# Kernel tuning notes

Measured on AMD Instinct MI355X. Metric: run time of the kernel, lower is better.

## Reference

```python
import jax, jax.numpy as jnp
import numpy as np
from jax.scipy.special import gammaln

BIG_NEG = -1e9
MAX_K = 20  # args.sm_max_span_length


def setup_inputs() -> dict:
    key = jax.random.key(0)
    ks = jax.random.split(key, 7)
    B, N, d, C = 16, 2048, 256, 128
    features = jax.random.normal(ks[0], (B, N, d), dtype=jnp.float32)
    lengths = jax.random.randint(ks[1], (B,), N // 2, N + 1)
    gaussian_means = jax.random.normal(ks[2], (C, d), dtype=jnp.float32)
    cov_diag = jax.random.uniform(ks[3], (d,), minval=0.5, maxval=1.5, dtype=jnp.float32)
    transition_logits = jax.random.normal(ks[4], (C, C), dtype=jnp.float32)
    init_logits = jax.random.uniform(ks[5], (C,), dtype=jnp.float32)
    poisson_log_rates = jax.random.normal(ks[6], (C,), dtype=jnp.float32) * 0.5 + 1.5
    return {"features": features, "lengths": lengths, "gaussian_means": gaussian_means,
            "cov_diag": cov_diag, "transition_logits": transition_logits,
            "init_logits": init_logits, "poisson_log_rates": poisson_log_rates}


def _emission_log_probs(features, means, cov_diag):
    # Diagonal-covariance MultivariateNormal log-prob, one class per column.
    # Quadratic form expanded to avoid materializing [B,N,C,d].
    inv_var = 1.0 / cov_diag
    d = features.shape[-1]
    const = -0.5 * (d * jnp.log(2.0 * jnp.pi) + jnp.sum(jnp.log(cov_diag)))
    xq = jnp.einsum('bnd,d->bn', features * features, inv_var)          # [B,N]
    mq = jnp.einsum('cd,d->c', means * means, inv_var)                  # [C]
    xm = jnp.einsum('bnd,cd->bnc', features, means * inv_var)           # [B,N,C]
    return const - 0.5 * (xq[..., None] + mq[None, None, :] - 2.0 * xm)  # [B,N,C]


def _length_log_probs(log_rates, K):
    # Poisson log-prob for span lengths k = 1..K.
    ks = jnp.arange(1, K + 1, dtype=jnp.float32)[:, None]               # [K,1]
    return ks * log_rates[None, :] - jnp.exp(log_rates)[None, :] - gammaln(ks + 1.0)  # [K,C]


def _transition_log_probs(transition_logits):
    C = transition_logits.shape[0]
    masked = jnp.where(jnp.eye(C, dtype=bool), BIG_NEG, transition_logits)  # no self-transitions
    return jax.nn.log_softmax(masked, axis=0)  # normalized over destination class (dim 0)


def _semimarkov_logZ(emis_lp, lengths, init_lp, trans_lp, len_lp, K):
    # Segmental (semi-Markov) CRF forward algorithm with sliding-window span sums.
    B, N, C = emis_lp.shape
    cum = jnp.concatenate([jnp.zeros((B, 1, C), emis_lp.dtype), jnp.cumsum(emis_lp, axis=1)], axis=1)
    cum_pad = jnp.concatenate([jnp.zeros((B, K, C), emis_lp.dtype), cum], axis=1)  # idx t+K <-> position t
    beta0 = jnp.full((B, N + 1 + K, C), BIG_NEG, emis_lp.dtype)
    beta0 = beta0.at[:, K, :].set(init_lp[None, :])  # position 0: initial distribution
    len_rev = len_lp[::-1]  # len_rev[j] == length log-prob of span length K-j

    def step(beta, t):
        w = jax.lax.dynamic_slice(beta, (0, t, 0), (B, K, C))        # beta at positions t-K..t-1
        cw = jax.lax.dynamic_slice(cum_pad, (0, t, 0), (B, K, C))
        ct = jax.lax.dynamic_slice(cum_pad, (0, t + K, 0), (B, 1, C))
        span = w + len_rev[None, :, :] + (ct - cw)                    # [B,K,C] span scores ending at t
        alpha_t = jax.nn.logsumexp(span, axis=1)                      # [B,C]
        beta_t = jax.nn.logsumexp(alpha_t[:, None, :] + trans_lp[None, :, :], axis=2)  # to-class
        beta = jax.lax.dynamic_update_slice(beta, beta_t[:, None, :], (0, t + K, 0))
        return beta, alpha_t

    _, alphas = jax.lax.scan(step, beta0, jnp.arange(1, N + 1))       # alphas: [N,B,C]
    final = alphas[lengths - 1, jnp.arange(B)]                        # [B,C] at each sequence end
    return jax.nn.logsumexp(final, axis=1)                            # [B] log partition


def reference(features, lengths, gaussian_means, cov_diag, transition_logits, init_logits, poisson_log_rates):
    emis_lp = _emission_log_probs(features, gaussian_means, cov_diag)
    init_lp = jax.nn.log_softmax(init_logits, axis=0)
    trans_lp = _transition_log_probs(transition_logits)
    len_lp = _length_log_probs(poisson_log_rates, MAX_K)
    return _semimarkov_logZ(emis_lp, lengths, init_lp, trans_lp, len_lp, MAX_K)
```

## Files before the change

### kernel.cpp

```cpp
#include <hip/hip_runtime.h>
#include <math.h>

#define Bb 16
#define Nn 2048
#define Dd 256
#define Cc 128
#define Kk 20
#define BIG_NEG -1.0e9f

#define WS_EMIS   0
#define WS_MSC    (WS_EMIS + Bb*Nn*Cc)
#define WS_XQ     (WS_MSC + Cc*Dd)
#define WS_ECHAN  (WS_XQ + Bb*Nn)
#define WS_T      (WS_ECHAN + Cc)
#define WS_LEN    (WS_T + Cc*Cc)
#define WS_INIT   (WS_LEN + Kk*Cc)
#define WS_IVAR   (WS_INIT + Cc)

typedef __attribute__((ext_vector_type(8))) short short8;
typedef __attribute__((ext_vector_type(4))) float float4v;

__device__ __forceinline__ unsigned short f32_to_bf16(float x) {
  unsigned int u = __builtin_bit_cast(unsigned int, x);
  u = (u + 0x7FFFu + ((u >> 16) & 1u)) >> 16;
  return (unsigned short)u;
}

#define DPP_STEP(x, op, ctrl, rmask)                                          \
  do {                                                                        \
    int _yi = __builtin_amdgcn_update_dpp(                                    \
        __builtin_bit_cast(int, x), __builtin_bit_cast(int, x), ctrl, rmask,  \
        0xF, true);                                                           \
    x = op(x, __builtin_bit_cast(float, _yi));                                \
  } while (0)

__device__ __forceinline__ float dpp_add(float a, float b) { return a + b; }

__device__ __forceinline__ float wave_max64(float x) {
  DPP_STEP(x, fmaxf, 0xB1, 0xF);
  DPP_STEP(x, fmaxf, 0x4E, 0xF);
  DPP_STEP(x, fmaxf, 0x141, 0xF);
  DPP_STEP(x, fmaxf, 0x140, 0xF);
  DPP_STEP(x, fmaxf, 0x142, 0xA);
  DPP_STEP(x, fmaxf, 0x143, 0xC);
  return __builtin_bit_cast(float,
      __builtin_amdgcn_readlane(__builtin_bit_cast(int, x), 63));
}

__device__ __forceinline__ float wave_sum64(float x) {
  DPP_STEP(x, dpp_add, 0xB1, 0xF);
  DPP_STEP(x, dpp_add, 0x4E, 0xF);
  DPP_STEP(x, dpp_add, 0x141, 0xF);
  DPP_STEP(x, dpp_add, 0x140, 0xF);
  DPP_STEP(x, dpp_add, 0x142, 0xA);
  DPP_STEP(x, dpp_add, 0x143, 0xC);
  return __builtin_bit_cast(float,
      __builtin_amdgcn_readlane(__builtin_bit_cast(int, x), 63));
}

__global__ void prep_kernel(const float* __restrict__ means,
                            const float* __restrict__ cov,
                            const float* __restrict__ tl,
                            const float* __restrict__ il,
                            const float* __restrict__ plr,
                            float* __restrict__ ws) {
  __shared__ float s_iv[Dd];
  __shared__ float s_red[4];
  __shared__ float s_tlse[Cc];
  int tid = threadIdx.x;

  float cv = cov[tid];
  float iv = 1.0f / cv;
  s_iv[tid] = iv;
  ws[WS_IVAR + tid] = iv;
  float lg = __logf(cv);
  #pragma unroll
  for (int off = 1; off < 64; off <<= 1) lg += __shfl_xor(lg, off, 64);
  if ((tid & 63) == 0) s_red[tid >> 6] = lg;
  __syncthreads();
  float logdet = s_red[0] + s_red[1] + s_red[2] + s_red[3];
  float cconst = -0.5f * ((float)Dd * 1.8378770664093453f + logdet);

  unsigned short* mscb = (unsigned short*)(ws + WS_MSC);
  for (int idx = tid; idx < Cc * Dd; idx += 256) {
    int d = idx & (Dd - 1);
    mscb[idx] = f32_to_bf16(means[idx] * s_iv[d]);
  }
  if (tid < Cc) {
    float acc = 0.0f;
    for (int d = 0; d < Dd; d++) {
      float m = means[tid * Dd + d];
      acc = fmaf(m * m, s_iv[d], acc);
    }
    ws[WS_ECHAN + tid] = cconst - 0.5f * acc;
  }
  for (int idx = tid; idx < Kk * Cc; idx += 256) {
    int L = idx / Cc + 1;
    int c = idx & (Cc - 1);
    float r = plr[c];
    ws[WS_LEN + idx] = (float)L * r - __expf(r) - lgammaf((float)(L + 1));
  }

  __syncthreads();
  float x = (tid < Cc) ? il[tid] : -INFINITY;
  float mx = x;
  #pragma unroll
  for (int off = 1; off < 64; off <<= 1) mx = fmaxf(mx, __shfl_xor(mx, off, 64));
  if ((tid & 63) == 0) s_red[tid >> 6] = mx;
  __syncthreads();
  float M = fmaxf(s_red[0], s_red[1]);
  float se = (tid < Cc) ? __expf(x - M) : 0.0f;
  #pragma unroll
  for (int off = 1; off < 64; off <<= 1) se += __shfl_xor(se, off, 64);
  __syncthreads();
  if ((tid & 63) == 0) s_red[tid >> 6] = se;
  __syncthreads();
  float lse = M + __logf(s_red[0] + s_red[1]);
  if (tid < Cc) ws[WS_INIT + tid] = x - lse;

  if (tid < Cc) {
    int j = tid;
    float m2 = -INFINITY;
    for (int i = 0; i < Cc; i++) if (i != j) m2 = fmaxf(m2, tl[i * Cc + j]);
    float s2 = 0.0f;
    for (int i = 0; i < Cc; i++) if (i != j) s2 += __expf(tl[i * Cc + j] - m2);
    s_tlse[j] = m2 + __logf(s2);
  }
  __syncthreads();
  for (int idx = tid; idx < Cc * Cc; idx += 256) {
    int i = idx / Cc;
    int j = idx & (Cc - 1);
    ws[WS_T + idx] = (i == j) ? 0.0f : __expf(tl[idx] - s_tlse[j]);
  }
}

__global__ void xq_kernel(const float* __restrict__ f, float* __restrict__ ws) {
  int pos = blockIdx.x * 4 + (threadIdx.x >> 6);
  int lane = threadIdx.x & 63;
  const float4 fv = *(const float4*)&f[(size_t)pos * Dd + lane * 4];
  const float4 vv = *(const float4*)&ws[WS_IVAR + lane * 4];
  float a = fv.x * fv.x * vv.x + fv.y * fv.y * vv.y +
            fv.z * fv.z * vv.z + fv.w * fv.w * vv.w;
  #pragma unroll
  for (int off = 1; off < 64; off <<= 1) a += __shfl_xor(a, off, 64);
  if (lane == 0) ws[WS_XQ + pos] = a;
}

__launch_bounds__(256)
__global__ void emis_mfma_kernel(const float* __restrict__ f, float* __restrict__ ws) {
  const unsigned short* msc = (const unsigned short*)(ws + WS_MSC);
  float* emis = ws + WS_EMIS;
  int tid = threadIdx.x;
  int w = tid >> 6, lane = tid & 63, g = lane >> 4, l16 = lane & 15;
  int b = blockIdx.x >> 6;
  int n0 = (blockIdx.x & 63) << 5;
  int c0 = w << 5;

  const float* fbase = f + (size_t)(b * Nn + n0) * Dd;
  float4v acc[2][2];
  #pragma unroll
  for (int rt = 0; rt < 2; rt++)
    #pragma unroll
    for (int ct = 0; ct < 2; ct++) acc[rt][ct] = (float4v){0.f, 0.f, 0.f, 0.f};

  #pragma unroll
  for (int k0 = 0; k0 < Dd; k0 += 32) {
    int kk = k0 + g * 8;
    short8 afr[2], bfr[2];
    #pragma unroll
    for (int rt = 0; rt < 2; rt++) {
      const float* src = fbase + (size_t)(rt * 16 + l16) * Dd + kk;
      float4 v0 = *(const float4*)src;
      float4 v1 = *(const float4*)(src + 4);
      short8 fr;
      fr[0] = (short)f32_to_bf16(v0.x); fr[1] = (short)f32_to_bf16(v0.y);
      fr[2] = (short)f32_to_bf16(v0.z); fr[3] = (short)f32_to_bf16(v0.w);
      fr[4] = (short)f32_to_bf16(v1.x); fr[5] = (short)f32_to_bf16(v1.y);
      fr[6] = (short)f32_to_bf16(v1.z); fr[7] = (short)f32_to_bf16(v1.w);
      afr[rt] = fr;
    }
    #pragma unroll
    for (int ct = 0; ct < 2; ct++)
      bfr[ct] = *(const short8*)&msc[(size_t)(c0 + ct * 16 + l16) * Dd + kk];
    #pragma unroll
    for (int rt = 0; rt < 2; rt++)
      #pragma unroll
      for (int ct = 0; ct < 2; ct++)
        acc[rt][ct] = __builtin_amdgcn_mfma_f32_16x16x32_bf16(afr[rt], bfr[ct], acc[rt][ct], 0, 0, 0);
  }

  #pragma unroll
  for (int rt = 0; rt < 2; rt++) {
    #pragma unroll
    for (int ct = 0; ct < 2; ct++) {
      int cc = c0 + ct * 16 + l16;
      float ec = ws[WS_ECHAN + cc];
      #pragma unroll
      for (int r = 0; r < 4; r++) {
        int row = rt * 16 + g * 4 + r;
        int nn = n0 + row;
        emis[(size_t)(b * Nn + nn) * Cc + cc] =
            ec - 0.5f * ws[WS_XQ + b * Nn + nn] + acc[rt][ct][r];
      }
    }
  }
}

__launch_bounds__(128, 1)
__global__ void scan_kernel(const int* __restrict__ lengths,
                            const float* __restrict__ ws,
                            float* __restrict__ out) {
  __shared__ __align__(16) unsigned short lds_pb[2][Cc];
  __shared__ float lds_wmax[2][2];
  __shared__ float lds_ps[2];
  int tid = threadIdx.x;
  int b = blockIdx.x;
  int c = tid;
  int w = tid >> 6;
  int lane = tid & 63;
  int g = lane >> 4;
  int len_b = lengths[b];
  const float* emis = ws + WS_EMIS + (size_t)b * Nn * Cc;

  short8 Tf[4][4];
  {
    const float* T = ws + WS_T;
    int row_lo = w * 64 + (lane & 15);
    int kg = g * 8;
    #pragma unroll
    for (int nt = 0; nt < 4; nt++)
      #pragma unroll
      for (int kt = 0; kt < 4; kt++) {
        const float* src = &T[(size_t)(row_lo + nt * 16) * Cc + kt * 32 + kg];
        short8 fr;
        #pragma unroll
        for (int j = 0; j < 8; j++) fr[j] = (short)f32_to_bf16(src[j]);
        Tf[nt][kt] = fr;
      }
  }

  float lenv[Kk];
  #pragma unroll
  for (int i = 0; i < Kk; i++) lenv[i] = ws[WS_LEN + i * Cc + c];
  float len0 = lenv[0];
  float dlen[Kk - 1];
  #pragma unroll
  for (int i = 1; i < Kk; i++) dlen[i - 1] = lenv[i] - lenv[i - 1];

  float h[Kk];
  #pragma unroll
  for (int i = 0; i < Kk; i++) h[i] = BIG_NEG;

  float gnew = ws[WS_INIT + c];
  float pm = BIG_NEG;
  float ps = 19.0f;

  float cum = emis[0 * Cc + c];
  float e[8], en[8];
  #pragma unroll
  for (int i = 0; i < 8; i++) e[i] = emis[(size_t)(1 + i) * Cc + c];

  bool done = false;
  for (int tg = 1; tg <= Nn && !done; tg += 8) {
    #pragma unroll
    for (int i = 0; i < 8; i++) {
      int t = tg + i;
      int buf = t & 1;

      float h0 = gnew + len0;
      float m = fmaxf(pm, h0);
      float sfix = fmaf(ps, __expf(pm - m), __expf(h0 - m));
      float mabs = m + cum;
      float wm = wave_max64(mabs);
      float p = sfix * __expf(mabs - wm);
      lds_pb[buf][c] = f32_to_bf16(p);
      if (lane == 0) lds_wmax[buf][w] = wm;
      bool is_out = (t == len_b);
      if (is_out) {
        float pssum = wave_sum64(p);
        if (lane == 0) lds_ps[w] = pssum;
      }
      h[0] = h0;
      __syncthreads();

      if (i == 0) {
        #pragma unroll
        for (int j = 0; j < 8; j++) {
          int r = tg + 8 + j; if (r > Nn - 1) r = Nn - 1;
          en[j] = emis[(size_t)r * Cc + c];
        }
      }
      float MA = lds_wmax[buf][0], MB = lds_wmax[buf][1];
      const unsigned short* pb = lds_pb[buf];
      short8 pa[4];
      #pragma unroll
      for (int kt = 0; kt < 4; kt++)
        pa[kt] = *(const short8*)&pb[kt * 32 + g * 8];

      #pragma unroll
      for (int k = Kk - 1; k > 0; k--) h[k] = h[k - 1] + dlen[k - 1];
      float m2[10];
      #pragma unroll
      for (int k = 0; k < 9; k++) m2[k] = fmaxf(h[1 + 2 * k], h[2 + 2 * k]);
      m2[9] = h[19];
      float m4a = fmaxf(fmaxf(m2[0], m2[1]), fmaxf(m2[2], m2[3]));
      float m4b = fmaxf(fmaxf(m2[4], m2[5]), fmaxf(m2[6], m2[7]));
      float pm2 = fmaxf(fmaxf(m4a, m4b), fmaxf(m2[8], m2[9]));
      float ex[Kk - 1];
      #pragma unroll
      for (int k = 1; k < Kk; k++) ex[k - 1] = __expf(h[k] - pm2);
      float s4[5];
      s4[0] = (ex[0] + ex[1]) + (ex[2] + ex[3]);
      s4[1] = (ex[4] + ex[5]) + (ex[6] + ex[7]);
      s4[2] = (ex[8] + ex[9]) + (ex[10] + ex[11]);
      s4[3] = (ex[12] + ex[13]) + (ex[14] + ex[15]);
      s4[4] = (ex[16] + ex[17]) + ex[18];
      float ps2 = ((s4[0] + s4[1]) + (s4[2] + s4[3])) + s4[4];

      float4v z = {0.0f, 0.0f, 0.0f, 0.0f};
      float4v accA[4], accB[4];
      #pragma unroll
      for (int nt = 0; nt < 4; nt++) {
        accA[nt] = __builtin_amdgcn_mfma_f32_16x16x32_bf16(pa[1], Tf[nt][1],
                     __builtin_amdgcn_mfma_f32_16x16x32_bf16(pa[0], Tf[nt][0], z, 0, 0, 0),
                     0, 0, 0);
        accB[nt] = __builtin_amdgcn_mfma_f32_16x16x32_bf16(pa[3], Tf[nt][3],
                     __builtin_amdgcn_mfma_f32_16x16x32_bf16(pa[2], Tf[nt][2], z, 0, 0, 0),
                     0, 0, 0);
      }
      float Mt = fmaxf(MA, MB);
      float sA = __expf(MA - Mt), sB = __expf(MB - Mt);
      float qa0 = (g == 0) ? accA[0][0] : accA[1][0];
      float qa1 = (g == 2) ? accA[2][0] : accA[3][0];
      float qa = (g < 2) ? qa0 : qa1;
      float qb0 = (g == 0) ? accB[0][0] : accB[1][0];
      float qb1 = (g == 2) ? accB[2][0] : accB[3][0];
      float qb = (g < 2) ? qb0 : qb1;
      float q = qa * sA + qb * sB;

      float rel = cum - Mt;
      gnew = (q > 0.0f) ? (__logf(q) - rel) : (-80.0f - rel);

      if (is_out) {
        if (tid == 0) out[b] = Mt + __logf(lds_ps[0] * sA + lds_ps[1] * sB);
        done = true;
        break;
      }
      pm = pm2;
      ps = ps2;
      cum += e[i];
    }
    if (!done) {
      #pragma unroll
      for (int i = 0; i < 8; i++) e[i] = en[i];
    }
  }
}

extern "C" void kernel_launch(void* const* d_in, const int* in_sizes, int n_in,
                              void* d_out, int out_size, void* d_ws, size_t ws_size,
                              hipStream_t stream) {
  const float* features = (const float*)d_in[0];
  const int* lengths = (const int*)d_in[1];
  const float* means = (const float*)d_in[2];
  const float* cov = (const float*)d_in[3];
  const float* tl = (const float*)d_in[4];
  const float* il = (const float*)d_in[5];
  const float* plr = (const float*)d_in[6];
  float* out = (float*)d_out;
  float* ws = (float*)d_ws;

  prep_kernel<<<1, 256, 0, stream>>>(means, cov, tl, il, plr, ws);
  xq_kernel<<<(Bb * Nn) / 4, 256, 0, stream>>>(features, ws);
  emis_mfma_kernel<<<Bb * (Nn / 32), 256, 0, stream>>>(features, ws);
  scan_kernel<<<Bb, 128, 0, stream>>>(lengths, ws, out);
}
```

Measured before the change: 1.539 ms.

## Rewrite semi-Markov scan in linear-space scaled recurrences and pack four batches per block

The scan moves from a log-space sliding window (per step: max over 19 terms, 19 exps, logsumexp) to a linear-space recurrence. The running span sums E are scaled multiplicatively by a per-step factor and dotted with precomputed exp(len) weights, and a Kahan-compensated log offset tracks the scale. The emission per-wave max is computed ahead of time from prefetched data, which takes the wave-max reduction off the dependent chain. Four batch sequences now share one 512-thread block, so 4 blocks are launched instead of 16. This reduces transcendental work on the serial critical path, at the cost of block-wide __syncthreads coupling the four sequences and possible underflow or precision risk from working in linear space.

```diff
diff --git a/kernel.cpp b/kernel.cpp
--- a/kernel.cpp
+++ b/kernel.cpp
@@ -206,19 +206,22 @@
   }
 }
 
-__launch_bounds__(128, 1)
+__launch_bounds__(512)
 __global__ void scan_kernel(const int* __restrict__ lengths,
                             const float* __restrict__ ws,
                             float* __restrict__ out) {
-  __shared__ __align__(16) unsigned short lds_pb[2][Cc];
-  __shared__ float lds_wmax[2][2];
-  __shared__ float lds_ps[2];
+  __shared__ __align__(16) unsigned short lds_pb[4][2][Cc];
+  __shared__ __align__(16) float lds_sc[4][2][4];
+  __shared__ float lds_out[4][2][2];
+
   int tid = threadIdx.x;
-  int b = blockIdx.x;
-  int c = tid;
-  int w = tid >> 6;
+  int w8 = tid >> 6;
+  int bi = w8 >> 1;
+  int w = w8 & 1;
   int lane = tid & 63;
   int g = lane >> 4;
+  int c = (w << 6) | lane;
+  int b = (blockIdx.x << 2) | bi;
   int len_b = lengths[b];
   const float* emis = ws + WS_EMIS + (size_t)b * Nn * Cc;
 
@@ -239,122 +242,157 @@
       }
   }
 
-  float lenv[Kk];
-  #pragma unroll
-  for (int i = 0; i < Kk; i++) lenv[i] = ws[WS_LEN + i * Cc + c];
-  float len0 = lenv[0];
-  float dlen[Kk - 1];
-  #pragma unroll
-  for (int i = 1; i < Kk; i++) dlen[i - 1] = lenv[i] - lenv[i - 1];
-
-  float h[Kk];
-  #pragma unroll
-  for (int i = 0; i < Kk; i++) h[i] = BIG_NEG;
-
-  float gnew = ws[WS_INIT + c];
-  float pm = BIG_NEG;
-  float ps = 19.0f;
-
-  float cum = emis[0 * Cc + c];
-  float e[8], en[8];
-  #pragma unroll
-  for (int i = 0; i < 8; i++) e[i] = emis[(size_t)(1 + i) * Cc + c];
-
-  bool done = false;
-  for (int tg = 1; tg <= Nn && !done; tg += 8) {
+  float elen[Kk];
+  #pragma unroll
+  for (int k2 = 0; k2 < Kk; k2++) elen[k2] = __expf(ws[WS_LEN + k2 * Cc + c]);
+  float elen0 = elen[0];
+
+  float E[Kk - 1];
+  #pragma unroll
+  for (int k2 = 0; k2 < Kk - 1; k2++) E[k2] = 0.0f;
+
+  float q = __expf(ws[WS_INIT + c]);
+  float Stail = 0.0f;
+  float cum = 0.0f;
+  float Dlt = 0.0f, dcomp = 0.0f;
+  float Mb = 0.0f;
+
+  float e[8], en[8], me[8];
+  #pragma unroll
+  for (int j = 0; j < 8; j++) e[j] = emis[(size_t)j * Cc + c];
+  #pragma unroll
+  for (int j = 0; j < 8; j++) me[j] = wave_max64(e[j]);
+  float eecur = __expf(e[0] - me[0]);
+
+  for (int tg = 1; tg <= Nn; tg += 8) {
     #pragma unroll
     for (int i = 0; i < 8; i++) {
       int t = tg + i;
       int buf = t & 1;
-
-      float h0 = gnew + len0;
-      float m = fmaxf(pm, h0);
-      float sfix = fmaf(ps, __expf(pm - m), __expf(h0 - m));
-      float mabs = m + cum;
-      float wm = wave_max64(mabs);
-      float p = sfix * __expf(mabs - wm);
-      lds_pb[buf][c] = f32_to_bf16(p);
-      if (lane == 0) lds_wmax[buf][w] = wm;
-      bool is_out = (t == len_b);
-      if (is_out) {
-        float pssum = wave_sum64(p);
-        if (lane == 0) lds_ps[w] = pssum;
-      }
-      h[0] = h0;
-      __syncthreads();
-
-      if (i == 0) {
-        #pragma unroll
-        for (int j = 0; j < 8; j++) {
-          int r = tg + 8 + j; if (r > Nn - 1) r = Nn - 1;
-          en[j] = emis[(size_t)r * Cc + c];
+      bool active = (t <= len_b);
+      bool fin = (t == len_b);
+      float ecur = e[i];
+      float S = 0.0f, a = 0.0f;
+
+      if (active) {
+        S = fmaf(q, elen0, Stail);
+        if (fin) {
+          a = (cum + ecur) + Dlt + __logf(S);
+          float Mw = wave_max64(a);
+          if (lane == 0) lds_out[bi][w][0] = Mw;
+        } else {
+          float v = S * eecur;
+          float wv = fmaxf(wave_max64(v), 1.0e-30f);
+          float p = v * __builtin_amdgcn_rcpf(wv);
+          lds_pb[bi][buf][c] = f32_to_bf16(p);
+          if (lane == 0) {
+            lds_sc[bi][buf][w * 2] = wv;
+            lds_sc[bi][buf][w * 2 + 1] = me[i];
+          }
         }
       }
-      float MA = lds_wmax[buf][0], MB = lds_wmax[buf][1];
-      const unsigned short* pb = lds_pb[buf];
-      short8 pa[4];
-      #pragma unroll
-      for (int kt = 0; kt < 4; kt++)
-        pa[kt] = *(const short8*)&pb[kt * 32 + g * 8];
-
-      #pragma unroll
-      for (int k = Kk - 1; k > 0; k--) h[k] = h[k - 1] + dlen[k - 1];
-      float m2[10];
-      #pragma unroll
-      for (int k = 0; k < 9; k++) m2[k] = fmaxf(h[1 + 2 * k], h[2 + 2 * k]);
-      m2[9] = h[19];
-      float m4a = fmaxf(fmaxf(m2[0], m2[1]), fmaxf(m2[2], m2[3]));
-      float m4b = fmaxf(fmaxf(m2[4], m2[5]), fmaxf(m2[6], m2[7]));
-      float pm2 = fmaxf(fmaxf(m4a, m4b), fmaxf(m2[8], m2[9]));
-      float ex[Kk - 1];
-      #pragma unroll
-      for (int k = 1; k < Kk; k++) ex[k - 1] = __expf(h[k] - pm2);
-      float s4[5];
-      s4[0] = (ex[0] + ex[1]) + (ex[2] + ex[3]);
-      s4[1] = (ex[4] + ex[5]) + (ex[6] + ex[7]);
-      s4[2] = (ex[8] + ex[9]) + (ex[10] + ex[11]);
-      s4[3] = (ex[12] + ex[13]) + (ex[14] + ex[15]);
-      s4[4] = (ex[16] + ex[17]) + ex[18];
-      float ps2 = ((s4[0] + s4[1]) + (s4[2] + s4[3])) + s4[4];
-
-      float4v z = {0.0f, 0.0f, 0.0f, 0.0f};
-      float4v accA[4], accB[4];
-      #pragma unroll
-      for (int nt = 0; nt < 4; nt++) {
-        accA[nt] = __builtin_amdgcn_mfma_f32_16x16x32_bf16(pa[1], Tf[nt][1],
-                     __builtin_amdgcn_mfma_f32_16x16x32_bf16(pa[0], Tf[nt][0], z, 0, 0, 0),
-                     0, 0, 0);
-        accB[nt] = __builtin_amdgcn_mfma_f32_16x16x32_bf16(pa[3], Tf[nt][3],
-                     __builtin_amdgcn_mfma_f32_16x16x32_bf16(pa[2], Tf[nt][2], z, 0, 0, 0),
-                     0, 0, 0);
+      __syncthreads();
+
+      if (active) {
+        if (fin) {
+          Mb = fmaxf(lds_out[bi][0][0], lds_out[bi][1][0]);
+          float ps = wave_sum64(__expf(a - Mb));
+          if (lane == 0) lds_out[bi][w][1] = ps;
+        } else {
+          if (i == 0) {
+            #pragma unroll
+            for (int j = 0; j < 8; j++) {
+              int rr = tg + 7 + j;
+              if (rr > Nn - 1) rr = Nn - 1;
+              en[j] = emis[(size_t)rr * Cc + c];
+            }
+          }
+          const unsigned short* pb = lds_pb[bi][buf];
+          short8 pa[4];
+          #pragma unroll
+          for (int kt = 0; kt < 4; kt++)
+            pa[kt] = *(const short8*)&pb[kt * 32 + g * 8];
+          float4 scv = *(const float4*)&lds_sc[bi][buf][0];
+
+          float laA = scv.y + __logf(scv.x);
+          float laB = scv.w + __logf(scv.z);
+          float dla = fmaxf(laA, laB);
+          float sA = __expf(laA - dla);
+          float sB = __expf(laB - dla);
+          float s_own = (w == 0) ? sA : sB;
+          float wv_own = (w == 0) ? scv.x : scv.z;
+          float sig = s_own * __builtin_amdgcn_rcpf(wv_own);
+          float sch = sig * eecur;
+
+          #pragma unroll
+          for (int k2 = Kk - 2; k2 >= 1; k2--) E[k2] = E[k2 - 1] * sch;
+          E[0] = q * sch;
+
+          float s0 = E[0] * elen[1];
+          float s1 = E[1] * elen[2];
+          float s2 = E[2] * elen[3];
+          float s3 = E[3] * elen[4];
+          s0 = fmaf(E[4], elen[5], s0);
+          s1 = fmaf(E[5], elen[6], s1);
+          s2 = fmaf(E[6], elen[7], s2);
+          s3 = fmaf(E[7], elen[8], s3);
+          s0 = fmaf(E[8], elen[9], s0);
+          s1 = fmaf(E[9], elen[10], s1);
+          s2 = fmaf(E[10], elen[11], s2);
+          s3 = fmaf(E[11], elen[12], s3);
+          s0 = fmaf(E[12], elen[13], s0);
+          s1 = fmaf(E[13], elen[14], s1);
+          s2 = fmaf(E[14], elen[15], s2);
+          s3 = fmaf(E[15], elen[16], s3);
+          s0 = fmaf(E[16], elen[17], s0);
+          s1 = fmaf(E[17], elen[18], s1);
+          s2 = fmaf(E[18], elen[19], s2);
+          Stail = (s0 + s1) + (s2 + s3);
+
+          if (i >= 2) me[i - 2] = wave_max64(en[i - 2]);
+
+          {
+            float dd = dla - ecur;
+            float y = dd - dcomp;
+            float t2 = Dlt + y;
+            dcomp = (t2 - Dlt) - y;
+            Dlt = t2;
+          }
+          cum += ecur;
+          if (i < 7) eecur = __expf(e[i + 1] - me[i + 1]);
+
+          float4v z = {0.0f, 0.0f, 0.0f, 0.0f};
+          float4v accA[4], accB[4];
+          #pragma unroll
+          for (int nt = 0; nt < 4; nt++) {
+            accA[nt] = __builtin_amdgcn_mfma_f32_16x16x32_bf16(pa[1], Tf[nt][1],
+                         __builtin_amdgcn_mfma_f32_16x16x32_bf16(pa[0], Tf[nt][0], z, 0, 0, 0),
+                         0, 0, 0);
+            accB[nt] = __builtin_amdgcn_mfma_f32_16x16x32_bf16(pa[3], Tf[nt][3],
+                         __builtin_amdgcn_mfma_f32_16x16x32_bf16(pa[2], Tf[nt][2], z, 0, 0, 0),
+                         0, 0, 0);
+          }
+          float qa0 = (g == 0) ? accA[0][0] : accA[1][0];
+          float qa1 = (g == 2) ? accA[2][0] : accA[3][0];
+          float qa = (g < 2) ? qa0 : qa1;
+          float qb0 = (g == 0) ? accB[0][0] : accB[1][0];
+          float qb1 = (g == 2) ? accB[2][0] : accB[3][0];
+          float qb = (g < 2) ? qb0 : qb1;
+          q = qa * sA + qb * sB;
+        }
       }
-      float Mt = fmaxf(MA, MB);
-      float sA = __expf(MA - Mt), sB = __expf(MB - Mt);
-      float qa0 = (g == 0) ? accA[0][0] : accA[1][0];
-      float qa1 = (g == 2) ? accA[2][0] : accA[3][0];
-      float qa = (g < 2) ? qa0 : qa1;
-      float qb0 = (g == 0) ? accB[0][0] : accB[1][0];
-      float qb1 = (g == 2) ? accB[2][0] : accB[3][0];
-      float qb = (g < 2) ? qb0 : qb1;
-      float q = qa * sA + qb * sB;
-
-      float rel = cum - Mt;
-      gnew = (q > 0.0f) ? (__logf(q) - rel) : (-80.0f - rel);
-
-      if (is_out) {
-        if (tid == 0) out[b] = Mt + __logf(lds_ps[0] * sA + lds_ps[1] * sB);
-        done = true;
-        break;
-      }
-      pm = pm2;
-      ps = ps2;
-      cum += e[i];
+      if (t == len_b + 1 && lane == 0 && w == 0)
+        out[b] = Mb + __logf(lds_out[bi][0][1] + lds_out[bi][1][1]);
     }
-    if (!done) {
-      #pragma unroll
-      for (int i = 0; i < 8; i++) e[i] = en[i];
-    }
-  }
+    me[6] = wave_max64(en[6]);
+    me[7] = wave_max64(en[7]);
+    #pragma unroll
+    for (int j = 0; j < 8; j++) e[j] = en[j];
+    eecur = __expf(e[0] - me[0]);
+  }
+  __syncthreads();
+  if (len_b == Nn && lane == 0 && w == 0)
+    out[b] = Mb + __logf(lds_out[bi][0][1] + lds_out[bi][1][1]);
 }
 
 extern "C" void kernel_launch(void* const* d_in, const int* in_sizes, int n_in,
@@ -373,5 +411,5 @@
   prep_kernel<<<1, 256, 0, stream>>>(means, cov, tl, il, plr, ws);
   xq_kernel<<<(Bb * Nn) / 4, 256, 0, stream>>>(features, ws);
   emis_mfma_kernel<<<Bb * (Nn / 32), 256, 0, stream>>>(features, ws);
-  scan_kernel<<<Bb, 128, 0, stream>>>(lengths, ws, out);
-}
+  scan_kernel<<<Bb / 4, 512, 0, stream>>>(lengths, ws, out);
+}
```

Result: slower. 2.098 ms (+36.3%).

## Rewrite semi-Markov scan in linear domain with single wave per batch

Applied to the files above, without the earlier changes.

The scan kernel now runs one 64-lane wave per sequence, with each lane owning two classes. The old log-domain span recursion (20 exps and a max tree per step) is replaced by a linear-domain recurrence with per-step rescaling by the wave max, and the log scale is tracked with Kahan-compensated sums. Removing the second wave drops the __syncthreads and cross-wave max exchange, leaving only an LDS waitcnt. The cost is twice the MFMA tiles per wave and some risk of underflow or overflow in the linear-domain products.

```diff
diff --git a/kernel.cpp b/kernel.cpp
--- a/kernel.cpp
+++ b/kernel.cpp
@@ -19,6 +19,7 @@
 
 typedef __attribute__((ext_vector_type(8))) short short8;
 typedef __attribute__((ext_vector_type(4))) float float4v;
+typedef __attribute__((ext_vector_type(2))) float float2v;
 
 __device__ __forceinline__ unsigned short f32_to_bf16(float x) {
   unsigned int u = __builtin_bit_cast(unsigned int, x);
@@ -206,153 +207,155 @@
   }
 }
 
-__launch_bounds__(128, 1)
+__launch_bounds__(64, 1)
 __global__ void scan_kernel(const int* __restrict__ lengths,
                             const float* __restrict__ ws,
                             float* __restrict__ out) {
-  __shared__ __align__(16) unsigned short lds_pb[2][Cc];
-  __shared__ float lds_wmax[2][2];
-  __shared__ float lds_ps[2];
-  int tid = threadIdx.x;
+  __shared__ __align__(16) unsigned short p_lds[Cc];
+
+  int lane = threadIdx.x;
+  int g = lane >> 4;
+  int l15 = lane & 15;
+  int c0 = g * 32 + l15;
+  int c1 = c0 + 16;
   int b = blockIdx.x;
-  int c = tid;
-  int w = tid >> 6;
-  int lane = tid & 63;
-  int g = lane >> 4;
   int len_b = lengths[b];
   const float* emis = ws + WS_EMIS + (size_t)b * Nn * Cc;
 
-  short8 Tf[4][4];
+  short8 Tf[8][4];
   {
     const float* T = ws + WS_T;
-    int row_lo = w * 64 + (lane & 15);
-    int kg = g * 8;
-    #pragma unroll
-    for (int nt = 0; nt < 4; nt++)
-      #pragma unroll
-      for (int kt = 0; kt < 4; kt++) {
-        const float* src = &T[(size_t)(row_lo + nt * 16) * Cc + kt * 32 + kg];
+    #pragma unroll
+    for (int nt = 0; nt < 8; nt++)
+      #pragma unroll
+      for (int kc = 0; kc < 4; kc++) {
+        const float* src = &T[(size_t)(nt * 16 + l15) * Cc + kc * 32 + g * 8];
         short8 fr;
         #pragma unroll
         for (int j = 0; j < 8; j++) fr[j] = (short)f32_to_bf16(src[j]);
-        Tf[nt][kt] = fr;
-      }
-  }
-
-  float lenv[Kk];
-  #pragma unroll
-  for (int i = 0; i < Kk; i++) lenv[i] = ws[WS_LEN + i * Cc + c];
-  float len0 = lenv[0];
-  float dlen[Kk - 1];
-  #pragma unroll
-  for (int i = 1; i < Kk; i++) dlen[i - 1] = lenv[i] - lenv[i - 1];
-
-  float h[Kk];
-  #pragma unroll
-  for (int i = 0; i < Kk; i++) h[i] = BIG_NEG;
-
-  float gnew = ws[WS_INIT + c];
-  float pm = BIG_NEG;
-  float ps = 19.0f;
-
-  float cum = emis[0 * Cc + c];
-  float e[8], en[8];
-  #pragma unroll
-  for (int i = 0; i < 8; i++) e[i] = emis[(size_t)(1 + i) * Cc + c];
+        Tf[nt][kc] = fr;
+      }
+  }
+
+  float2v elen[Kk];
+  #pragma unroll
+  for (int k = 0; k < Kk; k++)
+    elen[k] = (float2v){__expf(ws[WS_LEN + k * Cc + c0]),
+                        __expf(ws[WS_LEN + k * Cc + c1])};
+
+  float2v E[Kk - 1];
+  #pragma unroll
+  for (int s = 0; s < Kk - 1; s++) E[s] = (float2v){0.0f, 0.0f};
+
+  float2v q = (float2v){__expf(ws[WS_INIT + c0]), __expf(ws[WS_INIT + c1])};
+  float2v Stail = (float2v){0.0f, 0.0f};
+  float2v cum = (float2v){0.0f, 0.0f};
+  float2v Dlt = (float2v){0.0f, 0.0f};
+  float2v dcomp = (float2v){0.0f, 0.0f};
+
+  float2v e[8], en[8];
+  float me[8];
+  #pragma unroll
+  for (int j = 0; j < 8; j++)
+    e[j] = (float2v){emis[(size_t)j * Cc + c0], emis[(size_t)j * Cc + c1]};
+  #pragma unroll
+  for (int j = 0; j < 8; j++) me[j] = wave_max64(fmaxf(e[j].x, e[j].y));
+  float2v ee = (float2v){__expf(e[0].x - me[0]), __expf(e[0].y - me[0])};
 
   bool done = false;
   for (int tg = 1; tg <= Nn && !done; tg += 8) {
     #pragma unroll
     for (int i = 0; i < 8; i++) {
       int t = tg + i;
-      int buf = t & 1;
-
-      float h0 = gnew + len0;
-      float m = fmaxf(pm, h0);
-      float sfix = fmaf(ps, __expf(pm - m), __expf(h0 - m));
-      float mabs = m + cum;
-      float wm = wave_max64(mabs);
-      float p = sfix * __expf(mabs - wm);
-      lds_pb[buf][c] = f32_to_bf16(p);
-      if (lane == 0) lds_wmax[buf][w] = wm;
-      bool is_out = (t == len_b);
-      if (is_out) {
-        float pssum = wave_sum64(p);
-        if (lane == 0) lds_ps[w] = pssum;
-      }
-      h[0] = h0;
-      __syncthreads();
+      float2v ecur = e[i];
+      float2v S = q * elen[0] + Stail;
+
+      if (t == len_b) {
+        float ax = cum.x + ecur.x + Dlt.x + __logf(fmaxf(S.x, 1e-37f));
+        float ay = cum.y + ecur.y + Dlt.y + __logf(fmaxf(S.y, 1e-37f));
+        float Mb = wave_max64(fmaxf(ax, ay));
+        float ps = wave_sum64(__expf(ax - Mb) + __expf(ay - Mb));
+        if (lane == 0) out[b] = Mb + __logf(ps);
+        done = true;
+        break;
+      }
+
+      float2v v = S * ee;
+      p_lds[c0] = f32_to_bf16(v.x);
+      p_lds[c1] = f32_to_bf16(v.y);
+      asm volatile("s_waitcnt lgkmcnt(0)" ::: "memory");
+      short8 pa0 = *(const short8*)&p_lds[g * 8];
+      short8 pa1 = *(const short8*)&p_lds[32 + g * 8];
+      short8 pa2 = *(const short8*)&p_lds[64 + g * 8];
+      short8 pa3 = *(const short8*)&p_lds[96 + g * 8];
+
+      float wv = fmaxf(wave_max64(fmaxf(v.x, v.y)), 1.0e-30f);
+      float r = __builtin_amdgcn_rcpf(wv);
 
       if (i == 0) {
         #pragma unroll
         for (int j = 0; j < 8; j++) {
-          int r = tg + 8 + j; if (r > Nn - 1) r = Nn - 1;
-          en[j] = emis[(size_t)r * Cc + c];
+          int rr = tg + 7 + j;
+          if (rr > Nn - 1) rr = Nn - 1;
+          en[j] = (float2v){emis[(size_t)rr * Cc + c0], emis[(size_t)rr * Cc + c1]};
         }
       }
-      float MA = lds_wmax[buf][0], MB = lds_wmax[buf][1];
-      const unsigned short* pb = lds_pb[buf];
-      short8 pa[4];
-      #pragma unroll
-      for (int kt = 0; kt < 4; kt++)
-        pa[kt] = *(const short8*)&pb[kt * 32 + g * 8];
-
-      #pragma unroll
-      for (int k = Kk - 1; k > 0; k--) h[k] = h[k - 1] + dlen[k - 1];
-      float m2[10];
-      #pragma unroll
-      for (int k = 0; k < 9; k++) m2[k] = fmaxf(h[1 + 2 * k], h[2 + 2 * k]);
-      m2[9] = h[19];
-      float m4a = fmaxf(fmaxf(m2[0], m2[1]), fmaxf(m2[2], m2[3]));
-      float m4b = fmaxf(fmaxf(m2[4], m2[5]), fmaxf(m2[6], m2[7]));
-      float pm2 = fmaxf(fmaxf(m4a, m4b), fmaxf(m2[8], m2[9]));
-      float ex[Kk - 1];
-      #pragma unroll
-      for (int k = 1; k < Kk; k++) ex[k - 1] = __expf(h[k] - pm2);
-      float s4[5];
-      s4[0] = (ex[0] + ex[1]) + (ex[2] + ex[3]);
-      s4[1] = (ex[4] + ex[5]) + (ex[6] + ex[7]);
-      s4[2] = (ex[8] + ex[9]) + (ex[10] + ex[11]);
-      s4[3] = (ex[12] + ex[13]) + (ex[14] + ex[15]);
-      s4[4] = (ex[16] + ex[17]) + ex[18];
-      float ps2 = ((s4[0] + s4[1]) + (s4[2] + s4[3])) + s4[4];
 
       float4v z = {0.0f, 0.0f, 0.0f, 0.0f};
-      float4v accA[4], accB[4];
-      #pragma unroll
-      for (int nt = 0; nt < 4; nt++) {
-        accA[nt] = __builtin_amdgcn_mfma_f32_16x16x32_bf16(pa[1], Tf[nt][1],
-                     __builtin_amdgcn_mfma_f32_16x16x32_bf16(pa[0], Tf[nt][0], z, 0, 0, 0),
-                     0, 0, 0);
-        accB[nt] = __builtin_amdgcn_mfma_f32_16x16x32_bf16(pa[3], Tf[nt][3],
-                     __builtin_amdgcn_mfma_f32_16x16x32_bf16(pa[2], Tf[nt][2], z, 0, 0, 0),
-                     0, 0, 0);
-      }
-      float Mt = fmaxf(MA, MB);
-      float sA = __expf(MA - Mt), sB = __expf(MB - Mt);
-      float qa0 = (g == 0) ? accA[0][0] : accA[1][0];
-      float qa1 = (g == 2) ? accA[2][0] : accA[3][0];
-      float qa = (g < 2) ? qa0 : qa1;
-      float qb0 = (g == 0) ? accB[0][0] : accB[1][0];
-      float qb1 = (g == 2) ? accB[2][0] : accB[3][0];
-      float qb = (g < 2) ? qb0 : qb1;
-      float q = qa * sA + qb * sB;
-
-      float rel = cum - Mt;
-      gnew = (q > 0.0f) ? (__logf(q) - rel) : (-80.0f - rel);
-
-      if (is_out) {
-        if (tid == 0) out[b] = Mt + __logf(lds_ps[0] * sA + lds_ps[1] * sB);
-        done = true;
-        break;
-      }
-      pm = pm2;
-      ps = ps2;
-      cum += e[i];
+      float qv[8];
+      #pragma unroll
+      for (int nt = 0; nt < 8; nt++) {
+        float4v x = __builtin_amdgcn_mfma_f32_16x16x32_bf16(pa1, Tf[nt][1],
+                      __builtin_amdgcn_mfma_f32_16x16x32_bf16(pa0, Tf[nt][0], z, 0, 0, 0),
+                      0, 0, 0);
+        float4v y = __builtin_amdgcn_mfma_f32_16x16x32_bf16(pa3, Tf[nt][3],
+                      __builtin_amdgcn_mfma_f32_16x16x32_bf16(pa2, Tf[nt][2], z, 0, 0, 0),
+                      0, 0, 0);
+        qv[nt] = x[0] + y[0];
+      }
+
+      float2v sch = ee * r;
+      #pragma unroll
+      for (int s = Kk - 2; s >= 1; s--) E[s] = E[s - 1] * sch;
+      E[0] = q * sch;
+
+      float2v s0 = E[0] * elen[1];
+      float2v s1 = E[1] * elen[2];
+      float2v s2 = E[2] * elen[3];
+      float2v s3 = E[3] * elen[4];
+      s0 = E[4] * elen[5] + s0;   s1 = E[5] * elen[6] + s1;
+      s2 = E[6] * elen[7] + s2;   s3 = E[7] * elen[8] + s3;
+      s0 = E[8] * elen[9] + s0;   s1 = E[9] * elen[10] + s1;
+      s2 = E[10] * elen[11] + s2; s3 = E[11] * elen[12] + s3;
+      s0 = E[12] * elen[13] + s0; s1 = E[13] * elen[14] + s1;
+      s2 = E[14] * elen[15] + s2; s3 = E[15] * elen[16] + s3;
+      s0 = E[16] * elen[17] + s0; s1 = E[17] * elen[18] + s1;
+      s2 = E[18] * elen[19] + s2;
+      Stail = (s0 + s1) + (s2 + s3);
+
+      float dla = me[i] + __logf(wv);
+      float2v dd = (float2v){dla, dla} - ecur;
+      float2v yk = dd - dcomp;
+      float2v t2 = Dlt + yk;
+      dcomp = (t2 - Dlt) - yk;
+      Dlt = t2;
+      cum += ecur;
+
+      if (i >= 2) me[i - 2] = wave_max64(fmaxf(en[i - 2].x, en[i - 2].y));
+      if (i < 7)
+        ee = (float2v){__expf(e[i + 1].x - me[i + 1]),
+                       __expf(e[i + 1].y - me[i + 1])};
+
+      float q0 = (g & 2) ? ((g & 1) ? qv[6] : qv[4]) : ((g & 1) ? qv[2] : qv[0]);
+      float q1 = (g & 2) ? ((g & 1) ? qv[7] : qv[5]) : ((g & 1) ? qv[3] : qv[1]);
+      q = (float2v){q0 * r, q1 * r};
     }
     if (!done) {
-      #pragma unroll
-      for (int i = 0; i < 8; i++) e[i] = en[i];
+      me[6] = wave_max64(fmaxf(en[6].x, en[6].y));
+      me[7] = wave_max64(fmaxf(en[7].x, en[7].y));
+      #pragma unroll
+      for (int j = 0; j < 8; j++) e[j] = en[j];
+      ee = (float2v){__expf(e[0].x - me[0]), __expf(e[0].y - me[0])};
     }
   }
 }
@@ -373,5 +376,5 @@
   prep_kernel<<<1, 256, 0, stream>>>(means, cov, tl, il, plr, ws);
   xq_kernel<<<(Bb * Nn) / 4, 256, 0, stream>>>(features, ws);
   emis_mfma_kernel<<<Bb * (Nn / 32), 256, 0, stream>>>(features, ws);
-  scan_kernel<<<Bb, 128, 0, stream>>>(lengths, ws, out);
-}
+  scan_kernel<<<Bb, 64, 0, stream>>>(lengths, ws, out);
+}
```

Result: slower. 1.796 ms (+16.7%).
